# Kernel tuning notes

Measured on AMD Instinct MI355X. Metric: run time of the kernel, lower is better.

The kernel has to match this reference:

```python
import jax, jax.numpy as jnp
import numpy as np


def _lstm_layer(xs, Wih, Whh, b, h0, c0):
    # xs: [T, B, D] -> hs: [T, B, H]; PyTorch gate order i, f, g, o
    x_gates = jnp.einsum('tbd,gd->tbg', xs, Wih) + b  # precompute input projections

    def step(carry, xg):
        h, c = carry
        gates = xg + h @ Whh.T
        i, f, g, o = jnp.split(gates, 4, axis=-1)
        c = jax.nn.sigmoid(f) * c + jax.nn.sigmoid(i) * jnp.tanh(g)
        h = jax.nn.sigmoid(o) * jnp.tanh(c)
        return (h, c), h

    (h, c), hs = jax.lax.scan(step, (h0, c0), x_gates)
    return hs, h, c


def _stacked_lstm(xs, layer_params, init_states):
    # layer_params: list of (Wih, Whh, b); init_states: list of (h0, c0)
    finals = []
    h_seq = xs
    for (Wih, Whh, b), (h0, c0) in zip(layer_params, init_states):
        h_seq, h, c = _lstm_layer(h_seq, Wih, Whh, b, h0, c0)
        finals.append((h, c))
    return h_seq, finals


def setup_inputs() -> dict:
    key = jax.random.key(0)
    ks = jax.random.split(key, 20)
    B, T = 32, 128
    V, E, H = 32000, 512, 1024
    s = 0.05
    inp = {
        'x': jax.random.randint(ks[0], (B, T), 0, V, dtype=jnp.int64) if jax.config.read('jax_enable_x64') else jax.random.randint(ks[0], (B, T), 0, V, dtype=jnp.int32),
        'targets': jax.random.randint(ks[1], (B, T), 0, V, dtype=jnp.int32),
        'emb': jax.random.normal(ks[2], (V, E), jnp.float32) * s,
        'enc_Wih0': jax.random.normal(ks[3], (4 * H, E), jnp.float32) * s,
        'enc_Whh0': jax.random.normal(ks[4], (4 * H, H), jnp.float32) * s,
        'enc_b0': jax.random.normal(ks[5], (4 * H,), jnp.float32) * s,
        'enc_Wih1': jax.random.normal(ks[6], (4 * H, H), jnp.float32) * s,
        'enc_Whh1': jax.random.normal(ks[7], (4 * H, H), jnp.float32) * s,
        'enc_b1': jax.random.normal(ks[8], (4 * H,), jnp.float32) * s,
        'dec_Wih0': jax.random.normal(ks[9], (4 * H, E), jnp.float32) * s,
        'dec_Whh0': jax.random.normal(ks[10], (4 * H, H), jnp.float32) * s,
        'dec_b0': jax.random.normal(ks[11], (4 * H,), jnp.float32) * s,
        'dec_Wih1': jax.random.normal(ks[12], (4 * H, H), jnp.float32) * s,
        'dec_Whh1': jax.random.normal(ks[13], (4 * H, H), jnp.float32) * s,
        'dec_b1': jax.random.normal(ks[14], (4 * H,), jnp.float32) * s,
        'fc_W': jax.random.normal(ks[15], (V, H), jnp.float32) * s,
        'fc_b': jax.random.normal(ks[16], (V,), jnp.float32) * s,
    }
    return inp


def reference(x, targets, emb, enc_Wih0, enc_Whh0, enc_b0, enc_Wih1, enc_Whh1, enc_b1,
              dec_Wih0, dec_Whh0, dec_b0, dec_Wih1, dec_Whh1, dec_b1, fc_W, fc_b):
    B, T = x.shape
    H = enc_Whh0.shape[1]
    zero = jnp.zeros((B, H), emb.dtype)
    enc_params = [(enc_Wih0, enc_Whh0, enc_b0), (enc_Wih1, enc_Whh1, enc_b1)]
    dec_params = [(dec_Wih0, dec_Whh0, dec_b0), (dec_Wih1, dec_Whh1, dec_b1)]

    # Encoder (batch_first -> time-major for scan)
    enc_in = emb[x].transpose(1, 0, 2)  # [T, B, E]
    _, enc_finals = _stacked_lstm(enc_in, enc_params, [(zero, zero)] * 2)

    # Decoder with teacher forcing: input token 0 at t=0, then targets[:, t-1]
    dec_tok = jnp.concatenate([jnp.zeros((B, 1), targets.dtype), targets[:, :-1]], axis=1)
    dec_in = emb[dec_tok].transpose(1, 0, 2)  # [T, B, E]
    dec_hs, _ = _stacked_lstm(dec_in, dec_params, enc_finals)  # [T, B, H]

    logits = jnp.einsum('tbh,vh->btv', dec_hs, fc_W) + fc_b  # [B, T, V]
    return jax.nn.log_softmax(logits, axis=2)
```

## Files before the change

kernel.cpp:

```cpp
#include <hip/hip_runtime.h>


#define TSEQ  128
#define NB    32
#define EMB   512
#define HID   1024
#define G4    4096
#define VOC   32000
#define ROWS  (TSEQ * NB)
#define SCAN_BLOCKS 128

typedef __attribute__((ext_vector_type(8))) short short8;
typedef __attribute__((ext_vector_type(4))) float f32x4;

__device__ __forceinline__ unsigned short f2bf(float f) {
  unsigned u = __builtin_bit_cast(unsigned, f);
  u += 0x7FFFu + ((u >> 16) & 1u);
  return (unsigned short)(u >> 16);
}

__device__ __forceinline__ short8 pack8(float4 a, float4 b) {
  short8 v;
  v[0] = (short)f2bf(a.x); v[1] = (short)f2bf(a.y);
  v[2] = (short)f2bf(a.z); v[3] = (short)f2bf(a.w);
  v[4] = (short)f2bf(b.x); v[5] = (short)f2bf(b.y);
  v[6] = (short)f2bf(b.z); v[7] = (short)f2bf(b.w);
  return v;
}

__device__ __forceinline__ float fsig(float x)  { return 1.f / (1.f + __expf(-x)); }
__device__ __forceinline__ float ftanh(float x) { return 1.f - 2.f / (1.f + __expf(2.f * x)); }

__device__ __forceinline__ void async16(const void* g, void* l) {
  __builtin_amdgcn_global_load_lds((const __attribute__((address_space(1))) void*)g,
                                   (__attribute__((address_space(3))) void*)l, 16, 0, 0);
}

__global__ __launch_bounds__(256) void cvt_bf16(const float* __restrict__ src,
                                                unsigned short* __restrict__ dst, int n) {
  int i = (blockIdx.x * 256 + threadIdx.x) * 8;
  if (i >= n) return;
  float4 a = *(const float4*)&src[i];
  float4 b = *(const float4*)&src[i + 4];
  *(ushort4*)&dst[i]     = make_ushort4(f2bf(a.x), f2bf(a.y), f2bf(a.z), f2bf(a.w));
  *(ushort4*)&dst[i + 4] = make_ushort4(f2bf(b.x), f2bf(b.y), f2bf(b.z), f2bf(b.w));
}

__global__ __launch_bounds__(256) void gather_embed(const int* __restrict__ tok,
                                                    const float* __restrict__ emb,
                                                    unsigned short* __restrict__ dst, int dec) {
  int idx = blockIdx.x * 256 + threadIdx.x;
  int n = idx >> 7;
  int e = (idx & 127) * 4;
  int t = n >> 5, b = n & 31;
  int token;
  if (dec) token = (t == 0) ? 0 : tok[b * TSEQ + t - 1];
  else     token = tok[b * TSEQ + t];
  float4 v = *(const float4*)&emb[(size_t)token * EMB + e];
  *(ushort4*)&dst[(size_t)n * EMB + e] = make_ushort4(f2bf(v.x), f2bf(v.y), f2bf(v.z), f2bf(v.w));
}

__global__ __launch_bounds__(256) void zero_f(float* __restrict__ p, int n4) {
  for (int i = blockIdx.x * 256 + threadIdx.x; i < n4; i += gridDim.x * 256)
    ((float4*)p)[i] = make_float4(0.f, 0.f, 0.f, 0.f);
}

__global__ __launch_bounds__(256)
void gemm_bt(const unsigned short* __restrict__ A, const unsigned short* __restrict__ B,
             float* __restrict__ C, const float* __restrict__ bias,
             int M, int N, int K, int mode) {
  __shared__ short As[128 * 32];
  __shared__ short Bs[128 * 32];
  const int tid  = threadIdx.x;
  const int lane = tid & 63;
  const int wave = tid >> 6;
  const int m0 = blockIdx.y * 128, n0 = blockIdx.x * 128;
  const int wm = (wave >> 1) * 64, wn = (wave & 1) * 64;
  const int r = lane & 15, q = lane >> 4;

  f32x4 acc[4][4];
#pragma unroll
  for (int i = 0; i < 4; ++i)
#pragma unroll
    for (int j = 0; j < 4; ++j) acc[i][j] = (f32x4){0.f, 0.f, 0.f, 0.f};

  const int srow = tid >> 2;
  const int scol = (tid & 3) * 8;

  for (int k0 = 0; k0 < K; k0 += 32) {
    async16(&A[(size_t)(m0 + srow) * K + k0 + scol],      &As[tid * 8]);
    async16(&A[(size_t)(m0 + 64 + srow) * K + k0 + scol], &As[2048 + tid * 8]);
    async16(&B[(size_t)(n0 + srow) * K + k0 + scol],      &Bs[tid * 8]);
    async16(&B[(size_t)(n0 + 64 + srow) * K + k0 + scol], &Bs[2048 + tid * 8]);
    __builtin_amdgcn_s_waitcnt(0);
    __syncthreads();

    short8 af[4], bfr[4];
#pragma unroll
    for (int tm = 0; tm < 4; ++tm)
      af[tm] = *(const short8*)&As[(wm + tm * 16 + r) * 32 + q * 8];
#pragma unroll
    for (int tn = 0; tn < 4; ++tn)
      bfr[tn] = *(const short8*)&Bs[(wn + tn * 16 + r) * 32 + q * 8];
#pragma unroll
    for (int tm = 0; tm < 4; ++tm)
#pragma unroll
      for (int tn = 0; tn < 4; ++tn)
        acc[tm][tn] = __builtin_amdgcn_mfma_f32_16x16x32_bf16(af[tm], bfr[tn], acc[tm][tn], 0, 0, 0);
    __syncthreads();
  }

#pragma unroll
  for (int tm = 0; tm < 4; ++tm) {
#pragma unroll
    for (int tn = 0; tn < 4; ++tn) {
      f32x4 v = acc[tm][tn];
      int col = n0 + wn + tn * 16 + r;
      float bv = bias[col];
#pragma unroll
      for (int e = 0; e < 4; ++e) {
        int row = m0 + wm + tm * 16 + q * 4 + e;
        float val = v[e] + bv;
        size_t oidx;
        if (mode == 0) {
          oidx = (size_t)row * N + col;
        } else {
          int tt = row >> 5, bb = row & 31;
          oidx = (size_t)(bb * TSEQ + tt) * N + col;
        }
        C[oidx] = val;
      }
    }
  }
}

__global__ __launch_bounds__(256, 1)
void lstm_scan(const float* __restrict__ Whh, const float* __restrict__ xg,
               unsigned short* __restrict__ hA, unsigned short* __restrict__ hB,
               float* __restrict__ cbuf, unsigned short* __restrict__ hseq,
               unsigned* __restrict__ bar) {
  __shared__ float Gs[32][33];
  const int tid  = threadIdx.x;
  const int lane = tid & 63;
  const int wave = tid >> 6;
  const int r = lane & 15, q = lane >> 4;
  const int mt = wave >> 1, nt = wave & 1;
  const int D0 = blockIdx.x * 8;

  const int lr   = nt * 16 + r;
  const int grow = (lr >> 3) * HID + D0 + (lr & 7);
  short8 Bf[32];
  {
    const float* wp = &Whh[(size_t)grow * HID];
#pragma unroll
    for (int ks = 0; ks < 32; ++ks) {
      float4 w0 = *(const float4*)&wp[ks * 32 + q * 8];
      float4 w1 = *(const float4*)&wp[ks * 32 + q * 8 + 4];
      Bf[ks] = pack8(w0, w1);
    }
  }

  const int cd = tid & 7, cb = tid >> 3;
  float creg = cbuf[cb * HID + D0 + cd];

  for (int t = 0; t < TSEQ; ++t) {
    const unsigned short* hin  = (t & 1) ? hB : hA;
    unsigned short*       hout = (t & 1) ? hA : hB;

    const unsigned short* hrow = &hin[(size_t)(mt * 16 + r) * HID + q * 8];
    f32x4 a0 = (f32x4){0.f,0.f,0.f,0.f}, a1 = a0, a2 = a0, a3 = a0;
#pragma unroll
    for (int ks = 0; ks < 32; ks += 4) {
      a0 = __builtin_amdgcn_mfma_f32_16x16x32_bf16(*(const short8*)&hrow[(ks+0)*32], Bf[ks+0], a0, 0, 0, 0);
      a1 = __builtin_amdgcn_mfma_f32_16x16x32_bf16(*(const short8*)&hrow[(ks+1)*32], Bf[ks+1], a1, 0, 0, 0);
      a2 = __builtin_amdgcn_mfma_f32_16x16x32_bf16(*(const short8*)&hrow[(ks+2)*32], Bf[ks+2], a2, 0, 0, 0);
      a3 = __builtin_amdgcn_mfma_f32_16x16x32_bf16(*(const short8*)&hrow[(ks+3)*32], Bf[ks+3], a3, 0, 0, 0);
    }
    f32x4 acc = (a0 + a1) + (a2 + a3);
#pragma unroll
    for (int e = 0; e < 4; ++e)
      Gs[mt * 16 + q * 4 + e][nt * 16 + r] = acc[e];
    __syncthreads();

    const float* xrow = &xg[((size_t)t * NB + cb) * G4 + D0 + cd];
    float iv = Gs[cb][cd]      + xrow[0];
    float fv = Gs[cb][8 + cd]  + xrow[HID];
    float gv = Gs[cb][16 + cd] + xrow[2 * HID];
    float ov = Gs[cb][24 + cd] + xrow[3 * HID];
    float ig = fsig(iv), fg = fsig(fv), og = fsig(ov);
    float gg = ftanh(gv);
    creg = fg * creg + ig * gg;
    float hn = og * ftanh(creg);
    unsigned short hb = f2bf(hn);
    hout[cb * HID + D0 + cd] = hb;
    hseq[((size_t)t * NB + cb) * HID + D0 + cd] = hb;

    __syncthreads();
    if (tid == 0) {
      __threadfence();
      atomicAdd(bar, 1u);
      const unsigned target = (unsigned)(t + 1) * SCAN_BLOCKS;
      while (__hip_atomic_load(bar, __ATOMIC_RELAXED, __HIP_MEMORY_SCOPE_AGENT) < target)
        __builtin_amdgcn_s_sleep(2);
      __threadfence();
    }
    __syncthreads();
  }
  cbuf[cb * HID + D0 + cd] = creg;
}

__global__ __launch_bounds__(256) void logsoftmax_rows(float* __restrict__ out) {
  __shared__ float red[256];
  float* p = out + (size_t)blockIdx.x * VOC;
  const int tid = threadIdx.x;
  float m = -3.4e38f;
  for (int i = tid; i < VOC / 4; i += 256) {
    float4 v = ((const float4*)p)[i];
    m = fmaxf(m, fmaxf(fmaxf(v.x, v.y), fmaxf(v.z, v.w)));
  }
  red[tid] = m; __syncthreads();
  for (int s = 128; s; s >>= 1) { if (tid < s) red[tid] = fmaxf(red[tid], red[tid + s]); __syncthreads(); }
  float M = red[0]; __syncthreads();
  float sum = 0.f;
  for (int i = tid; i < VOC / 4; i += 256) {
    float4 v = ((const float4*)p)[i];
    sum += __expf(v.x - M) + __expf(v.y - M) + __expf(v.z - M) + __expf(v.w - M);
  }
  red[tid] = sum; __syncthreads();
  for (int s = 128; s; s >>= 1) { if (tid < s) red[tid] += red[tid + s]; __syncthreads(); }
  float L = M + logf(red[0]); __syncthreads();
  for (int i = tid; i < VOC / 4; i += 256) {
    float4 v = ((const float4*)p)[i];
    v.x -= L; v.y -= L; v.z -= L; v.w -= L;
    ((float4*)p)[i] = v;
  }
}

extern "C" void kernel_launch(void* const* d_in, const int* in_sizes, int n_in,
                              void* d_out, int out_size, void* d_ws, size_t ws_size,
                              hipStream_t stream) {
  const int*   x     = (const int*)  d_in[0];
  const int*   tgt   = (const int*)  d_in[1];
  const float* emb   = (const float*)d_in[2];
  const float* eWih0 = (const float*)d_in[3];
  const float* eWhh0 = (const float*)d_in[4];
  const float* eb0   = (const float*)d_in[5];
  const float* eWih1 = (const float*)d_in[6];
  const float* eWhh1 = (const float*)d_in[7];
  const float* eb1   = (const float*)d_in[8];
  const float* dWih0 = (const float*)d_in[9];
  const float* dWhh0 = (const float*)d_in[10];
  const float* db0   = (const float*)d_in[11];
  const float* dWih1 = (const float*)d_in[12];
  const float* dWhh1 = (const float*)d_in[13];
  const float* db1   = (const float*)d_in[14];
  const float* fcW   = (const float*)d_in[15];
  const float* fcb   = (const float*)d_in[16];
  float* out = (float*)d_out;

  char* base = (char*)d_ws;
  size_t off = 0;
  auto carve = [&](size_t bytes) -> void* {
    void* p = base + off;
    off += (bytes + 255) & ~(size_t)255;
    return p;
  };
  unsigned short* wE0   = (unsigned short*)carve((size_t)G4 * EMB * 2);
  unsigned short* wE1   = (unsigned short*)carve((size_t)G4 * HID * 2);
  unsigned short* wD0   = (unsigned short*)carve((size_t)G4 * EMB * 2);
  unsigned short* wD1   = (unsigned short*)carve((size_t)G4 * HID * 2);
  unsigned short* wFC   = (unsigned short*)carve((size_t)VOC * HID * 2);
  unsigned short* encin = (unsigned short*)carve((size_t)ROWS * EMB * 2);
  unsigned short* decin = (unsigned short*)carve((size_t)ROWS * EMB * 2);
  unsigned short* seqA  = (unsigned short*)carve((size_t)ROWS * HID * 2);
  unsigned short* seqB  = (unsigned short*)carve((size_t)ROWS * HID * 2);
  float* xg = (float*)carve((size_t)ROWS * G4 * 4);
  unsigned short* hA0 = (unsigned short*)carve((size_t)NB * HID * 2);
  unsigned short* hB0 = (unsigned short*)carve((size_t)NB * HID * 2);
  unsigned short* hA1 = (unsigned short*)carve((size_t)NB * HID * 2);
  unsigned short* hB1 = (unsigned short*)carve((size_t)NB * HID * 2);
  float* c0 = (float*)carve((size_t)NB * HID * 4);
  float* c1 = (float*)carve((size_t)NB * HID * 4);
  unsigned* bars = (unsigned*)carve(1024);
  const int zero_n4 = (4 * NB * HID * 2 + 2 * NB * HID * 4 + 1024) / 16;

  cvt_bf16<<<dim3(G4 * EMB / 2048), 256, 0, stream>>>(eWih0, wE0, G4 * EMB);
  cvt_bf16<<<dim3(G4 * HID / 2048), 256, 0, stream>>>(eWih1, wE1, G4 * HID);
  cvt_bf16<<<dim3(G4 * EMB / 2048), 256, 0, stream>>>(dWih0, wD0, G4 * EMB);
  cvt_bf16<<<dim3(G4 * HID / 2048), 256, 0, stream>>>(dWih1, wD1, G4 * HID);
  cvt_bf16<<<dim3(VOC * HID / 2048), 256, 0, stream>>>(fcW, wFC, VOC * HID);
  gather_embed<<<dim3(ROWS * EMB / 1024), 256, 0, stream>>>(x, emb, encin, 0);
  gather_embed<<<dim3(ROWS * EMB / 1024), 256, 0, stream>>>(tgt, emb, decin, 1);
  zero_f<<<dim3(128), 256, 0, stream>>>((float*)hA0, zero_n4);

  gemm_bt<<<dim3(G4 / 128, ROWS / 128), 256, 0, stream>>>(encin, wE0, xg, eb0, ROWS, G4, EMB, 0);
  lstm_scan<<<dim3(SCAN_BLOCKS), 256, 0, stream>>>(eWhh0, xg, hA0, hB0, c0, seqA, bars + 0);
  gemm_bt<<<dim3(G4 / 128, ROWS / 128), 256, 0, stream>>>(seqA, wE1, xg, eb1, ROWS, G4, HID, 0);
  lstm_scan<<<dim3(SCAN_BLOCKS), 256, 0, stream>>>(eWhh1, xg, hA1, hB1, c1, seqB, bars + 16);
  gemm_bt<<<dim3(G4 / 128, ROWS / 128), 256, 0, stream>>>(decin, wD0, xg, db0, ROWS, G4, EMB, 0);
  lstm_scan<<<dim3(SCAN_BLOCKS), 256, 0, stream>>>(dWhh0, xg, hA0, hB0, c0, seqA, bars + 32);
  gemm_bt<<<dim3(G4 / 128, ROWS / 128), 256, 0, stream>>>(seqA, wD1, xg, db1, ROWS, G4, HID, 0);
  lstm_scan<<<dim3(SCAN_BLOCKS), 256, 0, stream>>>(dWhh1, xg, hA1, hB1, c1, seqB, bars + 48);
  gemm_bt<<<dim3(VOC / 128, ROWS / 128), 256, 0, stream>>>(seqB, wFC, out, fcb, ROWS, VOC, HID, 1);
  logsoftmax_rows<<<dim3(ROWS), 256, 0, stream>>>(out);
}
```

Baseline: 8.829 ms.

## Fuse two LSTM layers into one wavefront-pipelined persistent scan kernel

Replaces the per-layer scan kernels and the between-layer input-projection GEMM with one persistent kernel that runs layer 0 at step s and layer 1 at step s-1 in the same iteration, sharing a single grid barrier. Layer 1's input projection is computed inside the scan using a swizzled LDS copy of its bf16 input weights, so the sequential time steps of both layers overlap and the intermediate sequence no longer goes through global memory. The cost is twice the MFMA work per step on only 128 blocks, 64 extra weight registers per thread, 64KB of LDS, and the loss of a fully parallel GEMM for layer 1's input projection.

```diff
diff --git a/kernel.cpp b/kernel.cpp
--- a/kernel.cpp
+++ b/kernel.cpp
@@ -135,11 +135,19 @@
 }
 
 __global__ __launch_bounds__(256, 1)
-void lstm_scan(const float* __restrict__ Whh, const float* __restrict__ xg,
-               unsigned short* __restrict__ hA, unsigned short* __restrict__ hB,
-               float* __restrict__ cbuf, unsigned short* __restrict__ hseq,
-               unsigned* __restrict__ bar) {
-  __shared__ float Gs[32][33];
+void lstm_scan2(const float* __restrict__ Whh0, const float* __restrict__ Whh1,
+                const unsigned short* __restrict__ Wih1,
+                const float* __restrict__ b1,
+                const float* __restrict__ xg,
+                unsigned short* __restrict__ h0A, unsigned short* __restrict__ h0B,
+                float* __restrict__ c0buf,
+                unsigned short* __restrict__ h1A, unsigned short* __restrict__ h1B,
+                float* __restrict__ c1buf,
+                unsigned short* __restrict__ hseq1, int write_seq,
+                unsigned* __restrict__ bar) {
+  __shared__ float Gs0[32][33];
+  __shared__ float Gs1[32][33];
+  __shared__ unsigned short Wlds[32 * 1024];
   const int tid  = threadIdx.x;
   const int lane = tid & 63;
   const int wave = tid >> 6;
@@ -149,64 +157,135 @@
 
   const int lr   = nt * 16 + r;
   const int grow = (lr >> 3) * HID + D0 + (lr & 7);
-  short8 Bf[32];
+  short8 Bf0[32], Bf1[32];
   {
-    const float* wp = &Whh[(size_t)grow * HID];
+    const float* wp0 = &Whh0[(size_t)grow * HID];
+    const float* wp1 = &Whh1[(size_t)grow * HID];
 #pragma unroll
     for (int ks = 0; ks < 32; ++ks) {
-      float4 w0 = *(const float4*)&wp[ks * 32 + q * 8];
-      float4 w1 = *(const float4*)&wp[ks * 32 + q * 8 + 4];
-      Bf[ks] = pack8(w0, w1);
-    }
+      Bf0[ks] = pack8(*(const float4*)&wp0[ks * 32 + q * 8],
+                      *(const float4*)&wp0[ks * 32 + q * 8 + 4]);
+      Bf1[ks] = pack8(*(const float4*)&wp1[ks * 32 + q * 8],
+                      *(const float4*)&wp1[ks * 32 + q * 8 + 4]);
+    }
+  }
+
+#pragma unroll
+  for (int i = 0; i < 16; ++i) {
+    int j   = i * 256 + tid;
+    int lr2 = j >> 7, c16 = j & 127;
+    int gr2 = (lr2 >> 3) * HID + D0 + (lr2 & 7);
+    short8 v = *(const short8*)&Wih1[(size_t)gr2 * HID + c16 * 8];
+    *(short8*)((char*)Wlds + lr2 * 2048 + ((c16 ^ (lr2 & 7)) * 16)) = v;
   }
 
   const int cd = tid & 7, cb = tid >> 3;
-  float creg = cbuf[cb * HID + D0 + cd];
-
-  for (int t = 0; t < TSEQ; ++t) {
-    const unsigned short* hin  = (t & 1) ? hB : hA;
-    unsigned short*       hout = (t & 1) ? hA : hB;
-
-    const unsigned short* hrow = &hin[(size_t)(mt * 16 + r) * HID + q * 8];
-    f32x4 a0 = (f32x4){0.f,0.f,0.f,0.f}, a1 = a0, a2 = a0, a3 = a0;
-#pragma unroll
-    for (int ks = 0; ks < 32; ks += 4) {
-      a0 = __builtin_amdgcn_mfma_f32_16x16x32_bf16(*(const short8*)&hrow[(ks+0)*32], Bf[ks+0], a0, 0, 0, 0);
-      a1 = __builtin_amdgcn_mfma_f32_16x16x32_bf16(*(const short8*)&hrow[(ks+1)*32], Bf[ks+1], a1, 0, 0, 0);
-      a2 = __builtin_amdgcn_mfma_f32_16x16x32_bf16(*(const short8*)&hrow[(ks+2)*32], Bf[ks+2], a2, 0, 0, 0);
-      a3 = __builtin_amdgcn_mfma_f32_16x16x32_bf16(*(const short8*)&hrow[(ks+3)*32], Bf[ks+3], a3, 0, 0, 0);
-    }
-    f32x4 acc = (a0 + a1) + (a2 + a3);
-#pragma unroll
-    for (int e = 0; e < 4; ++e)
-      Gs[mt * 16 + q * 4 + e][nt * 16 + r] = acc[e];
+  float creg0 = c0buf[cb * HID + D0 + cd];
+  float creg1 = c1buf[cb * HID + D0 + cd];
+  const float bi1 = b1[0 * HID + D0 + cd];
+  const float bf1 = b1[1 * HID + D0 + cd];
+  const float bg1 = b1[2 * HID + D0 + cd];
+  const float bo1 = b1[3 * HID + D0 + cd];
+  __syncthreads();
+
+  for (int s = 0; s <= TSEQ; ++s) {
+    const int t0c = (s < TSEQ) ? s : (TSEQ - 1);
+    const int t1c = (s >= 1) ? (s - 1) : 0;
+
+    const float* xrow = &xg[((size_t)t0c * NB + cb) * G4 + D0 + cd];
+    const float x_i = xrow[0];
+    const float x_f = xrow[HID];
+    const float x_g = xrow[2 * HID];
+    const float x_o = xrow[3 * HID];
+
+    {
+      const unsigned short* h0in = (t0c & 1) ? h0B : h0A;
+      const unsigned short* hrow = &h0in[(size_t)(mt * 16 + r) * HID + q * 8];
+      f32x4 a0 = (f32x4){0.f, 0.f, 0.f, 0.f}, a1 = a0, a2 = a0, a3 = a0;
+#pragma unroll
+      for (int ks = 0; ks < 32; ks += 4) {
+        a0 = __builtin_amdgcn_mfma_f32_16x16x32_bf16(*(const short8*)&hrow[(ks + 0) * 32], Bf0[ks + 0], a0, 0, 0, 0);
+        a1 = __builtin_amdgcn_mfma_f32_16x16x32_bf16(*(const short8*)&hrow[(ks + 1) * 32], Bf0[ks + 1], a1, 0, 0, 0);
+        a2 = __builtin_amdgcn_mfma_f32_16x16x32_bf16(*(const short8*)&hrow[(ks + 2) * 32], Bf0[ks + 2], a2, 0, 0, 0);
+        a3 = __builtin_amdgcn_mfma_f32_16x16x32_bf16(*(const short8*)&hrow[(ks + 3) * 32], Bf0[ks + 3], a3, 0, 0, 0);
+      }
+      f32x4 acc = (a0 + a1) + (a2 + a3);
+#pragma unroll
+      for (int e = 0; e < 4; ++e)
+        Gs0[mt * 16 + q * 4 + e][nt * 16 + r] = acc[e];
+    }
+
+    {
+      const unsigned short* h1in = (t1c & 1) ? h1B : h1A;
+      const unsigned short* h0t  = (t1c & 1) ? h0A : h0B;
+      const unsigned short* hrow1 = &h1in[(size_t)(mt * 16 + r) * HID + q * 8];
+      const unsigned short* hrowx = &h0t [(size_t)(mt * 16 + r) * HID + q * 8];
+      f32x4 a0 = (f32x4){0.f, 0.f, 0.f, 0.f}, a1 = a0, a2 = a0, a3 = a0;
+#pragma unroll
+      for (int ks = 0; ks < 32; ks += 4) {
+        a0 = __builtin_amdgcn_mfma_f32_16x16x32_bf16(*(const short8*)&hrow1[(ks + 0) * 32], Bf1[ks + 0], a0, 0, 0, 0);
+        a1 = __builtin_amdgcn_mfma_f32_16x16x32_bf16(*(const short8*)&hrow1[(ks + 1) * 32], Bf1[ks + 1], a1, 0, 0, 0);
+        a2 = __builtin_amdgcn_mfma_f32_16x16x32_bf16(*(const short8*)&hrow1[(ks + 2) * 32], Bf1[ks + 2], a2, 0, 0, 0);
+        a3 = __builtin_amdgcn_mfma_f32_16x16x32_bf16(*(const short8*)&hrow1[(ks + 3) * 32], Bf1[ks + 3], a3, 0, 0, 0);
+      }
+#pragma unroll
+      for (int ks = 0; ks < 32; ks += 4) {
+        short8 w0 = *(const short8*)((const char*)Wlds + lr * 2048 + ((((ks + 0) * 4 + q) ^ (lr & 7)) * 16));
+        short8 w1 = *(const short8*)((const char*)Wlds + lr * 2048 + ((((ks + 1) * 4 + q) ^ (lr & 7)) * 16));
+        short8 w2 = *(const short8*)((const char*)Wlds + lr * 2048 + ((((ks + 2) * 4 + q) ^ (lr & 7)) * 16));
+        short8 w3 = *(const short8*)((const char*)Wlds + lr * 2048 + ((((ks + 3) * 4 + q) ^ (lr & 7)) * 16));
+        a0 = __builtin_amdgcn_mfma_f32_16x16x32_bf16(*(const short8*)&hrowx[(ks + 0) * 32], w0, a0, 0, 0, 0);
+        a1 = __builtin_amdgcn_mfma_f32_16x16x32_bf16(*(const short8*)&hrowx[(ks + 1) * 32], w1, a1, 0, 0, 0);
+        a2 = __builtin_amdgcn_mfma_f32_16x16x32_bf16(*(const short8*)&hrowx[(ks + 2) * 32], w2, a2, 0, 0, 0);
+        a3 = __builtin_amdgcn_mfma_f32_16x16x32_bf16(*(const short8*)&hrowx[(ks + 3) * 32], w3, a3, 0, 0, 0);
+      }
+      f32x4 acc = (a0 + a1) + (a2 + a3);
+#pragma unroll
+      for (int e = 0; e < 4; ++e)
+        Gs1[mt * 16 + q * 4 + e][nt * 16 + r] = acc[e];
+    }
     __syncthreads();
 
-    const float* xrow = &xg[((size_t)t * NB + cb) * G4 + D0 + cd];
-    float iv = Gs[cb][cd]      + xrow[0];
-    float fv = Gs[cb][8 + cd]  + xrow[HID];
-    float gv = Gs[cb][16 + cd] + xrow[2 * HID];
-    float ov = Gs[cb][24 + cd] + xrow[3 * HID];
-    float ig = fsig(iv), fg = fsig(fv), og = fsig(ov);
-    float gg = ftanh(gv);
-    creg = fg * creg + ig * gg;
-    float hn = og * ftanh(creg);
-    unsigned short hb = f2bf(hn);
-    hout[cb * HID + D0 + cd] = hb;
-    hseq[((size_t)t * NB + cb) * HID + D0 + cd] = hb;
-
-    __syncthreads();
-    if (tid == 0) {
-      __threadfence();
-      atomicAdd(bar, 1u);
-      const unsigned target = (unsigned)(t + 1) * SCAN_BLOCKS;
-      while (__hip_atomic_load(bar, __ATOMIC_RELAXED, __HIP_MEMORY_SCOPE_AGENT) < target)
-        __builtin_amdgcn_s_sleep(2);
-      __threadfence();
-    }
-    __syncthreads();
-  }
-  cbuf[cb * HID + D0 + cd] = creg;
+    if (s < TSEQ) {
+      float iv = Gs0[cb][cd]      + x_i;
+      float fv = Gs0[cb][8 + cd]  + x_f;
+      float gv = Gs0[cb][16 + cd] + x_g;
+      float ov = Gs0[cb][24 + cd] + x_o;
+      float ig = fsig(iv), fg = fsig(fv), og = fsig(ov);
+      float gg = ftanh(gv);
+      creg0 = fg * creg0 + ig * gg;
+      float hn = og * ftanh(creg0);
+      ((t0c & 1) ? h0A : h0B)[cb * HID + D0 + cd] = f2bf(hn);
+    }
+    if (s >= 1) {
+      float iv = Gs1[cb][cd]      + bi1;
+      float fv = Gs1[cb][8 + cd]  + bf1;
+      float gv = Gs1[cb][16 + cd] + bg1;
+      float ov = Gs1[cb][24 + cd] + bo1;
+      float ig = fsig(iv), fg = fsig(fv), og = fsig(ov);
+      float gg = ftanh(gv);
+      creg1 = fg * creg1 + ig * gg;
+      float hn = og * ftanh(creg1);
+      unsigned short hb = f2bf(hn);
+      ((t1c & 1) ? h1A : h1B)[cb * HID + D0 + cd] = hb;
+      if (write_seq) hseq1[((size_t)t1c * NB + cb) * HID + D0 + cd] = hb;
+    }
+
+    if (s < TSEQ) {
+      __syncthreads();
+      if (tid == 0) {
+        __threadfence();
+        atomicAdd(bar, 1u);
+        const unsigned target = (unsigned)(s + 1) * SCAN_BLOCKS;
+        while (__hip_atomic_load(bar, __ATOMIC_RELAXED, __HIP_MEMORY_SCOPE_AGENT) < target)
+          __builtin_amdgcn_s_sleep(2);
+        __threadfence();
+      }
+      __syncthreads();
+    }
+  }
+  c0buf[cb * HID + D0 + cd] = creg0;
+  c1buf[cb * HID + D0 + cd] = creg1;
 }
 
 __global__ __launch_bounds__(256) void logsoftmax_rows(float* __restrict__ out) {
@@ -272,7 +351,6 @@
   unsigned short* wFC   = (unsigned short*)carve((size_t)VOC * HID * 2);
   unsigned short* encin = (unsigned short*)carve((size_t)ROWS * EMB * 2);
   unsigned short* decin = (unsigned short*)carve((size_t)ROWS * EMB * 2);
-  unsigned short* seqA  = (unsigned short*)carve((size_t)ROWS * HID * 2);
   unsigned short* seqB  = (unsigned short*)carve((size_t)ROWS * HID * 2);
   float* xg = (float*)carve((size_t)ROWS * G4 * 4);
   unsigned short* hA0 = (unsigned short*)carve((size_t)NB * HID * 2);
@@ -294,13 +372,13 @@
   zero_f<<<dim3(128), 256, 0, stream>>>((float*)hA0, zero_n4);
 
   gemm_bt<<<dim3(G4 / 128, ROWS / 128), 256, 0, stream>>>(encin, wE0, xg, eb0, ROWS, G4, EMB, 0);
-  lstm_scan<<<dim3(SCAN_BLOCKS), 256, 0, stream>>>(eWhh0, xg, hA0, hB0, c0, seqA, bars + 0);
-  gemm_bt<<<dim3(G4 / 128, ROWS / 128), 256, 0, stream>>>(seqA, wE1, xg, eb1, ROWS, G4, HID, 0);
-  lstm_scan<<<dim3(SCAN_BLOCKS), 256, 0, stream>>>(eWhh1, xg, hA1, hB1, c1, seqB, bars + 16);
+  lstm_scan2<<<dim3(SCAN_BLOCKS), 256, 0, stream>>>(eWhh0, eWhh1, wE1, eb1, xg,
+                                                    hA0, hB0, c0, hA1, hB1, c1,
+                                                    seqB, 0, bars + 0);
   gemm_bt<<<dim3(G4 / 128, ROWS / 128), 256, 0, stream>>>(decin, wD0, xg, db0, ROWS, G4, EMB, 0);
-  lstm_scan<<<dim3(SCAN_BLOCKS), 256, 0, stream>>>(dWhh0, xg, hA0, hB0, c0, seqA, bars + 32);
-  gemm_bt<<<dim3(G4 / 128, ROWS / 128), 256, 0, stream>>>(seqA, wD1, xg, db1, ROWS, G4, HID, 0);
-  lstm_scan<<<dim3(SCAN_BLOCKS), 256, 0, stream>>>(dWhh1, xg, hA1, hB1, c1, seqB, bars + 48);
+  lstm_scan2<<<dim3(SCAN_BLOCKS), 256, 0, stream>>>(dWhh0, dWhh1, wD1, db1, xg,
+                                                    hA0, hB0, c0, hA1, hB1, c1,
+                                                    seqB, 1, bars + 16);
   gemm_bt<<<dim3(VOC / 128, ROWS / 128), 256, 0, stream>>>(seqB, wFC, out, fcb, ROWS, VOC, HID, 1);
   logsoftmax_rows<<<dim3(ROWS), 256, 0, stream>>>(out);
 }
```

After: 8.470 ms. 1.04x faster.
